# Performance work log

Hardware: AMD Instinct MI355X
Metric: run time of the kernel (lower is better)

## Reference

```python
import jax, jax.numpy as jnp
import numpy as np

N, E, L, H, D, HID = 32768, 262144, 4, 8, 64, 512
IN_DIM, OUT_DIM, EDIM, MAX_SP = 386, 384, 32, 4


def setup_inputs() -> dict:
    key = jax.random.key(0)
    k = jax.random.split(key, 16)
    s = 0.02
    d = {}
    d["embeddings"] = jax.random.normal(k[0], (N, IN_DIM), jnp.float32)
    d["edge_index"] = jax.random.randint(k[1], (2, E), 0, N)
    d["edge_attr_ids"] = jax.random.randint(k[2], (E,), 0, MAX_SP)
    d["Win"] = jax.random.normal(k[3], (IN_DIM, HID)) * s
    d["bin_"] = jnp.zeros((HID,))
    d["Etab"] = jax.random.normal(k[4], (MAX_SP, EDIM)) * s
    d["Wq"] = jax.random.normal(k[5], (L, HID, HID)) * s
    d["bq"] = jnp.zeros((L, HID))
    d["Wk"] = jax.random.normal(k[6], (L, HID, HID)) * s
    d["bk"] = jnp.zeros((L, HID))
    d["Wv"] = jax.random.normal(k[7], (L, HID, HID)) * s
    d["bv"] = jnp.zeros((L, HID))
    d["We"] = jax.random.normal(k[8], (L, EDIM, HID)) * s
    d["be"] = jnp.zeros((L, HID))
    d["Ws"] = jax.random.normal(k[9], (L, HID, HID)) * s
    d["bs"] = jnp.zeros((L, HID))
    d["Wbeta"] = jax.random.normal(k[10], (L, 3 * HID, 1)) * s
    d["bbeta"] = jnp.zeros((L, 1))
    d["ln_g"] = jnp.ones((L, HID))
    d["ln_b"] = jnp.zeros((L, HID))
    d["Wout"] = jax.random.normal(k[11], (HID, OUT_DIM)) * s
    d["bout"] = jnp.zeros((OUT_DIM,))
    return d


def _ln(x, g, b):
    mu = x.mean(-1, keepdims=True)
    var = ((x - mu) ** 2).mean(-1, keepdims=True)
    return (x - mu) * jax.lax.rsqrt(var + 1e-5) * g + b


def _fwd(embeddings, edge_index, edge_attr_ids, Win, bin_, Etab, Wq, bq, Wk, bk,
         Wv, bv, We, be, Ws, bs, Wbeta, bbeta, ln_g, ln_b, Wout, bout):
    src, dst = edge_index[0], edge_index[1]  # messages flow src -> dst (PyG convention)
    h = embeddings @ Win + bin_              # [N, HID]
    e = Etab[edge_attr_ids]                  # [E, EDIM]
    scale = 1.0 / np.sqrt(D).astype(np.float32)
    for l in range(L):
        q = (h @ Wq[l] + bq[l]).reshape(N, H, D)
        kk = (h @ Wk[l] + bk[l]).reshape(N, H, D)
        v = (h @ Wv[l] + bv[l]).reshape(N, H, D)
        ee = (e @ We[l] + be[l]).reshape(E, H, D)
        kj = kk[src] + ee                    # [E, H, D]
        vj = v[src] + ee                     # [E, H, D]
        alpha = jnp.einsum('ehd,ehd->eh', q[dst], kj) * scale  # [E, H]
        # segment softmax over incoming edges of each target node
        amax = jax.lax.stop_gradient(jax.ops.segment_max(alpha, dst, num_segments=N))
        ex = jnp.exp(alpha - amax[dst])
        denom = jax.ops.segment_sum(ex, dst, num_segments=N)
        a = ex / denom[dst]                  # [E, H] (dropout in eval mode -> identity)
        out = jax.ops.segment_sum(a[..., None] * vj, dst, num_segments=N).reshape(N, HID)
        # beta-gated skip connection (PyG TransformerConv beta=True)
        xr = h @ Ws[l] + bs[l]
        beta = jax.nn.sigmoid(jnp.concatenate([out, xr, out - xr], axis=-1) @ Wbeta[l] + bbeta[l])
        out = beta * xr + (1.0 - beta) * out
        h = _ln(h + out, ln_g[l], ln_b[l])
    return h @ Wout + bout


def reference(embeddings, edge_index, edge_attr_ids, Win, bin_, Etab, Wq, bq, Wk,
              bk, Wv, bv, We, be, Ws, bs, Wbeta, bbeta, ln_g, ln_b, Wout, bout):
    return _fwd(embeddings, edge_index, edge_attr_ids, Win, bin_, Etab, Wq, bq,
                Wk, bk, Wv, bv, We, be, Ws, bs, Wbeta, bbeta, ln_g, ln_b, Wout, bout)
```

## Files before the change

### kernel.cpp

```cpp
#include <hip/hip_runtime.h>
#include <math.h>

#define NN      32768
#define EE_N    262144
#define LL      4
#define HID     512
#define IN_DIM  386
#define KP_IN   416
#define OUT_DIM 384
#define EDIM    32
#define MAX_SP  4
#define QKV_LD  1536

typedef __attribute__((ext_vector_type(8))) __bf16 bf16x8;
typedef __attribute__((ext_vector_type(4))) float  f32x4;

__device__ __forceinline__ unsigned short f2bf(float f) {
    unsigned int u = __float_as_uint(f);
    unsigned int r = (u + 0x7FFFu + ((u >> 16) & 1u)) >> 16;
    return (unsigned short)r;
}
__device__ __forceinline__ void unpack2(unsigned int w, float& lo, float& hi) {
    lo = __uint_as_float(w << 16);
    hi = __uint_as_float(w & 0xFFFF0000u);
}

template <int OUT_MODE>
__global__ __launch_bounds__(256) void gemm_mfma(
    const unsigned short* __restrict__ A,
    const unsigned short* __restrict__ Bt,
    const float* __restrict__ bias,
    void* __restrict__ C0, void* __restrict__ C1,
    int M, int Kp, int N, int ldc)
{
    __shared__ unsigned short As[128 * 32];
    __shared__ unsigned short Bs[128 * 32];

    const int t    = threadIdx.x;
    const int lane = t & 63, wid = t >> 6;
    const int wr   = wid >> 1, wc = wid & 1;

    const int nwg = gridDim.x * gridDim.y;
    int bid = blockIdx.y * gridDim.x + blockIdx.x;
    if ((nwg & 7) == 0) bid = (bid & 7) * (nwg >> 3) + (bid >> 3);
    const int row0 = (bid / gridDim.x) * 128;
    const int col0 = (bid % gridDim.x) * 128;

    f32x4 acc[4][4] = {};

    const int srow  = lane >> 2;
    const int sslot = lane & 3;
    const int kq    = lane >> 4;
    const int l15   = lane & 15;

    for (int kt = 0; kt < Kp; kt += 32) {
#pragma unroll
        for (int i = 0; i < 2; ++i) {
            const int rbase = wid * 32 + i * 16;
            {
                const int r    = rbase + srow;
                const int koff = sslot ^ ((r >> 1) & 3);
                const unsigned short* ga = &A[(size_t)(row0 + r) * Kp + kt + koff * 8];
                __builtin_amdgcn_global_load_lds(
                    (const __attribute__((address_space(1))) unsigned int*)ga,
                    (__attribute__((address_space(3))) unsigned int*)&As[rbase * 32],
                    16, 0, 0);
            }
            {
                const int c    = rbase + srow;
                const int koff = sslot ^ ((c >> 1) & 3);
                const unsigned short* gb = &Bt[(size_t)(col0 + c) * Kp + kt + koff * 8];
                __builtin_amdgcn_global_load_lds(
                    (const __attribute__((address_space(1))) unsigned int*)gb,
                    (__attribute__((address_space(3))) unsigned int*)&Bs[rbase * 32],
                    16, 0, 0);
            }
        }
        __syncthreads();

        bf16x8 af[4], bfr[4];
#pragma unroll
        for (int mi = 0; mi < 4; ++mi) {
            const int r    = wr * 64 + mi * 16 + l15;
            const int slot = kq ^ ((r >> 1) & 3);
            af[mi] = *reinterpret_cast<const bf16x8*>(&As[r * 32 + slot * 8]);
        }
#pragma unroll
        for (int ni = 0; ni < 4; ++ni) {
            const int c    = wc * 64 + ni * 16 + l15;
            const int slot = kq ^ ((c >> 1) & 3);
            bfr[ni] = *reinterpret_cast<const bf16x8*>(&Bs[c * 32 + slot * 8]);
        }
#pragma unroll
        for (int mi = 0; mi < 4; ++mi)
#pragma unroll
            for (int ni = 0; ni < 4; ++ni)
                acc[mi][ni] = __builtin_amdgcn_mfma_f32_16x16x32_bf16(
                    af[mi], bfr[ni], acc[mi][ni], 0, 0, 0);
        __syncthreads();
    }

    const int cb = col0 + wc * 64;
    const int rb = row0 + wr * 64;
    float bv[4];
#pragma unroll
    for (int ni = 0; ni < 4; ++ni) bv[ni] = bias[cb + ni * 16 + l15];

#pragma unroll
    for (int mi = 0; mi < 4; ++mi) {
#pragma unroll
        for (int ni = 0; ni < 4; ++ni) {
            const int col = cb + ni * 16 + l15;
#pragma unroll
            for (int r = 0; r < 4; ++r) {
                const int row = rb + mi * 16 + kq * 4 + r;
                const float oval = acc[mi][ni][r] + bv[ni];
                if (OUT_MODE == 0) {
                    ((float*)C0)[(size_t)row * ldc + col] = oval;
                } else if (OUT_MODE == 1) {
                    ((unsigned short*)C0)[(size_t)row * ldc + col] = f2bf(oval);
                } else {
                    ((float*)C0)[(size_t)row * ldc + col] = oval;
                    ((unsigned short*)C1)[(size_t)row * ldc + col] = f2bf(oval);
                }
            }
        }
    }
}

__global__ __launch_bounds__(256) void convert_wt(
    const float* __restrict__ W, unsigned short* __restrict__ Wt,
    int K, int N, int Kp)
{
    __shared__ float tile[32][33];
    const int tx = threadIdx.x, ty = threadIdx.y;
    const int kb = blockIdx.y * 32, nb = blockIdx.x * 32;
#pragma unroll
    for (int i = 0; i < 32; i += 8) {
        const int k = kb + ty + i, n = nb + tx;
        tile[ty + i][tx] = (k < K && n < N) ? W[(size_t)k * N + n] : 0.f;
    }
    __syncthreads();
#pragma unroll
    for (int i = 0; i < 32; i += 8) {
        const int n = nb + ty + i, k = kb + tx;
        if (n < N && k < Kp)
            Wt[(size_t)n * Kp + k] = f2bf(tile[tx][ty + i]);
    }
}

__global__ __launch_bounds__(256) void convert_wt_batch(
    const float* __restrict__ Wq, const float* __restrict__ Wk,
    const float* __restrict__ Wv, const float* __restrict__ Ws,
    unsigned short* __restrict__ Wlt)
{
    __shared__ float tile[32][33];
    const int m = blockIdx.z;
    const int l = m >> 2, tp = m & 3;
    const float* W = (tp == 0 ? Wq : tp == 1 ? Wk : tp == 2 ? Wv : Ws)
                     + (size_t)l * HID * HID;
    unsigned short* Wt = Wlt + (size_t)m * HID * HID;
    const int tx = threadIdx.x, ty = threadIdx.y;
    const int kb = blockIdx.y * 32, nb = blockIdx.x * 32;
#pragma unroll
    for (int i = 0; i < 32; i += 8)
        tile[ty + i][tx] = W[(size_t)(kb + ty + i) * HID + nb + tx];
    __syncthreads();
#pragma unroll
    for (int i = 0; i < 32; i += 8)
        Wt[(size_t)(nb + ty + i) * HID + kb + tx] = f2bf(tile[tx][ty + i]);
}

__global__ __launch_bounds__(256) void convert_emb(
    const float* __restrict__ emb, unsigned short* __restrict__ ebf)
{
    const int n = blockIdx.x;
    for (int k = threadIdx.x; k < KP_IN; k += 256)
        ebf[(size_t)n * KP_IN + k] =
            (k < IN_DIM) ? f2bf(emb[(size_t)n * IN_DIM + k]) : (unsigned short)0;
}

__global__ void ee_all_kernel(const float* __restrict__ Etab,
                              const float* __restrict__ We,
                              const float* __restrict__ be,
                              float* __restrict__ ee4)
{
    const int l = blockIdx.x, j = threadIdx.x;
    const float* Wel = We + (size_t)l * EDIM * HID;
    const float  bel = be[(size_t)l * HID + j];
    for (int a = 0; a < MAX_SP; ++a) {
        float s = bel;
        for (int kk = 0; kk < EDIM; ++kk)
            s = fmaf(Etab[a * EDIM + kk], Wel[(size_t)kk * HID + j], s);
        ee4[((size_t)l * MAX_SP + a) * HID + j] = s;
    }
}

__global__ void bias_fuse_kernel(const float* __restrict__ bq,
                                 const float* __restrict__ bk,
                                 const float* __restrict__ bv,
                                 float* __restrict__ bqkv)
{
    const int i = blockIdx.x * 256 + threadIdx.x;
    const int l = i / QKV_LD, r = i % QKV_LD;
    float val = (r < 512) ? bq[l * 512 + r]
              : (r < 1024) ? bk[l * 512 + r - 512]
                           : bv[l * 512 + r - 1024];
    bqkv[i] = val;
}

__global__ void hist_kernel(const int* __restrict__ dst, int* __restrict__ deg)
{
    int e = blockIdx.x * blockDim.x + threadIdx.x;
    if (e < EE_N) atomicAdd(&deg[dst[e]], 1);
}

__global__ __launch_bounds__(1024) void scan_kernel(
    const int* __restrict__ deg, int* __restrict__ row_ptr, int* __restrict__ cursor)
{
    __shared__ int sdata[1024];
    const int t = threadIdx.x;
    const int base = t * 32;
    int s = 0;
    for (int i = 0; i < 32; ++i) s += deg[base + i];
    sdata[t] = s;
    __syncthreads();
    for (int off = 1; off < 1024; off <<= 1) {
        int val = (t >= off) ? sdata[t - off] : 0;
        __syncthreads();
        sdata[t] += val;
        __syncthreads();
    }
    int run = sdata[t] - s;
    for (int i = 0; i < 32; ++i) {
        row_ptr[base + i] = run;
        cursor[base + i]  = run;
        run += deg[base + i];
    }
    if (t == 1023) row_ptr[NN] = run;
}

__global__ void scatter_kernel(const int* __restrict__ src, const int* __restrict__ dst,
                               const int* __restrict__ aid, int* __restrict__ cursor,
                               int* __restrict__ csr_pack)
{
    int e = blockIdx.x * blockDim.x + threadIdx.x;
    if (e < EE_N) {
        int d = dst[e];
        int pos = atomicAdd(&cursor[d], 1);
        csr_pack[pos] = src[e] | (aid[e] << 16);
    }
}

__global__ __launch_bounds__(256) void attn_kernel(
    unsigned short* __restrict__ qkv, const float* __restrict__ ee,
    const int* __restrict__ row_ptr, const int* __restrict__ csr_pack)
{
    __shared__ float ees[MAX_SP * HID];
    const int t = threadIdx.x;
    for (int i = t; i < MAX_SP * HID; i += 256) ees[i] = ee[i];
    __syncthreads();

    const int wave = t >> 6, lane = t & 63;
    const int node = blockIdx.x * 4 + wave;
    const int off  = lane << 3;

    float qa[8];
    {
        uint4 qv = *reinterpret_cast<const uint4*>(&qkv[(size_t)node * QKV_LD + off]);
        unpack2(qv.x, qa[0], qa[1]); unpack2(qv.y, qa[2], qa[3]);
        unpack2(qv.z, qa[4], qa[5]); unpack2(qv.w, qa[6], qa[7]);
    }

    float denom = 0.f;
    float acc[8] = {0.f, 0.f, 0.f, 0.f, 0.f, 0.f, 0.f, 0.f};

    const int beg = row_ptr[node], end = row_ptr[node + 1];
    for (int i = beg; i < end; ++i) {
        const int p   = csr_pack[i];
        const int s   = p & 0xFFFF;
        const int aid = p >> 16;
        const float* ep = &ees[aid * HID + off];
        const unsigned short* kp = &qkv[(size_t)s * QKV_LD + 512 + off];

        uint4 kv = *reinterpret_cast<const uint4*>(kp);
        uint4 vv = *reinterpret_cast<const uint4*>(kp + 512);

        float kj[8];
        unpack2(kv.x, kj[0], kj[1]); unpack2(kv.y, kj[2], kj[3]);
        unpack2(kv.z, kj[4], kj[5]); unpack2(kv.w, kj[6], kj[7]);
        float partial = 0.f;
#pragma unroll
        for (int j = 0; j < 8; ++j) partial = fmaf(qa[j], kj[j] + ep[j], partial);
        partial += __shfl_xor(partial, 1);
        partial += __shfl_xor(partial, 2);
        partial += __shfl_xor(partial, 4);
        const float w = __expf(partial * 0.125f);
        denom += w;

        float vj[8];
        unpack2(vv.x, vj[0], vj[1]); unpack2(vv.y, vj[2], vj[3]);
        unpack2(vv.z, vj[4], vj[5]); unpack2(vv.w, vj[6], vj[7]);
#pragma unroll
        for (int j = 0; j < 8; ++j) acc[j] = fmaf(w, vj[j] + ep[j], acc[j]);
    }

    const float inv = (denom > 0.f) ? (1.f / denom) : 0.f;
    union { unsigned short us[8]; uint4 v4; } pk;
#pragma unroll
    for (int j = 0; j < 8; ++j) pk.us[j] = f2bf(acc[j] * inv);
    *reinterpret_cast<uint4*>(&qkv[(size_t)node * QKV_LD + off]) = pk.v4;
}

__global__ __launch_bounds__(256) void blend_ln_kernel(
    float* __restrict__ h, unsigned short* __restrict__ hbf,
    const unsigned short* __restrict__ qkv, const float* __restrict__ wbeta,
    const float* __restrict__ bbeta, const float* __restrict__ ln_g,
    const float* __restrict__ ln_b)
{
    const int t = threadIdx.x;
    const int wave = t >> 6, lane = t & 63;
    const int node = blockIdx.x * 4 + wave;
    const int off  = lane << 3;

    float o8[8], x8[8], h8[8];
    {
        uint4 a = *reinterpret_cast<const uint4*>(&qkv[(size_t)node * QKV_LD + off]);
        unpack2(a.x, o8[0], o8[1]); unpack2(a.y, o8[2], o8[3]);
        unpack2(a.z, o8[4], o8[5]); unpack2(a.w, o8[6], o8[7]);
        uint4 b = *reinterpret_cast<const uint4*>(&qkv[(size_t)node * QKV_LD + 512 + off]);
        unpack2(b.x, x8[0], x8[1]); unpack2(b.y, x8[2], x8[3]);
        unpack2(b.z, x8[4], x8[5]); unpack2(b.w, x8[6], x8[7]);
        float4 c0 = *reinterpret_cast<const float4*>(&h[(size_t)node * HID + off]);
        float4 c1 = *reinterpret_cast<const float4*>(&h[(size_t)node * HID + off + 4]);
        h8[0]=c0.x; h8[1]=c0.y; h8[2]=c0.z; h8[3]=c0.w; h8[4]=c1.x; h8[5]=c1.y; h8[6]=c1.z; h8[7]=c1.w;
    }

    float p = 0.f;
#pragma unroll
    for (int j = 0; j < 8; ++j) {
        float w1 = wbeta[off + j];
        float w2 = wbeta[HID + off + j];
        float w3 = wbeta[2 * HID + off + j];
        p = fmaf(o8[j], w1 + w3, p);
        p = fmaf(x8[j], w2 - w3, p);
    }
#pragma unroll
    for (int m = 1; m <= 32; m <<= 1) p += __shfl_xor(p, m);
    const float beta = 1.f / (1.f + __expf(-(p + bbeta[0])));

    float y[8];
    float s = 0.f;
#pragma unroll
    for (int j = 0; j < 8; ++j) {
        y[j] = h8[j] + beta * x8[j] + (1.f - beta) * o8[j];
        s += y[j];
    }
#pragma unroll
    for (int m = 1; m <= 32; m <<= 1) s += __shfl_xor(s, m);
    const float mean = s * (1.f / HID);

    float vs = 0.f;
#pragma unroll
    for (int j = 0; j < 8; ++j) {
        float d = y[j] - mean;
        vs = fmaf(d, d, vs);
    }
#pragma unroll
    for (int m = 1; m <= 32; m <<= 1) vs += __shfl_xor(vs, m);
    const float rstd = rsqrtf(vs * (1.f / HID) + 1e-5f);

    float rr[8];
    union { unsigned short us[8]; uint4 v4; } pk;
#pragma unroll
    for (int j = 0; j < 8; ++j) {
        rr[j] = (y[j] - mean) * rstd * ln_g[off + j] + ln_b[off + j];
        pk.us[j] = f2bf(rr[j]);
    }
    float4 r0 = {rr[0], rr[1], rr[2], rr[3]};
    float4 r1 = {rr[4], rr[5], rr[6], rr[7]};
    *reinterpret_cast<float4*>(&h[(size_t)node * HID + off])     = r0;
    *reinterpret_cast<float4*>(&h[(size_t)node * HID + off + 4]) = r1;
    *reinterpret_cast<uint4*>(&hbf[(size_t)node * HID + off])    = pk.v4;
}

extern "C" void kernel_launch(void* const* d_in, const int* in_sizes, int n_in,
                              void* d_out, int out_size, void* d_ws, size_t ws_size,
                              hipStream_t stream)
{
    (void)in_sizes; (void)n_in; (void)out_size; (void)ws_size;
    const float* emb   = (const float*)d_in[0];
    const int*   eidx  = (const int*)d_in[1];
    const int*   aid   = (const int*)d_in[2];
    const float* Win   = (const float*)d_in[3];
    const float* bin_  = (const float*)d_in[4];
    const float* Etab  = (const float*)d_in[5];
    const float* Wq    = (const float*)d_in[6];
    const float* bq    = (const float*)d_in[7];
    const float* Wk    = (const float*)d_in[8];
    const float* bk    = (const float*)d_in[9];
    const float* Wv    = (const float*)d_in[10];
    const float* bv    = (const float*)d_in[11];
    const float* We    = (const float*)d_in[12];
    const float* be    = (const float*)d_in[13];
    const float* Ws    = (const float*)d_in[14];
    const float* bs    = (const float*)d_in[15];
    const float* Wbeta = (const float*)d_in[16];
    const float* bbeta = (const float*)d_in[17];
    const float* ln_g  = (const float*)d_in[18];
    const float* ln_b  = (const float*)d_in[19];
    const float* Wout  = (const float*)d_in[20];
    const float* bout  = (const float*)d_in[21];
    float* out = (float*)d_out;

    char* w = (char*)d_ws;
    float* h            = (float*)w;           w += (size_t)NN * HID * 4;
    unsigned short* hbf = (unsigned short*)w;  w += (size_t)NN * HID * 2;
    unsigned short* qkv = (unsigned short*)w;  w += (size_t)NN * QKV_LD * 2;
    unsigned short* embbf = qkv;
    unsigned short* Winbf  = (unsigned short*)w; w += (size_t)HID * KP_IN * 2;
    unsigned short* Wlt    = (unsigned short*)w; w += (size_t)16 * HID * HID * 2;
    unsigned short* Woutbf = (unsigned short*)w; w += (size_t)OUT_DIM * HID * 2;
    float* ee4   = (float*)w;  w += (size_t)LL * MAX_SP * HID * 4;
    float* bqkv  = (float*)w;  w += (size_t)LL * QKV_LD * 4;
    int* row_ptr = (int*)w;    w += (NN + 4) * 4;
    int* cursor  = (int*)w;    w += NN * 4;
    int* deg     = (int*)w;    w += NN * 4;
    int* csr_pack = (int*)w;   w += EE_N * 4;

    const int* src = eidx;
    const int* dst = eidx + EE_N;

    hipMemsetAsync(deg, 0, NN * sizeof(int), stream);
    hist_kernel<<<EE_N / 256, 256, 0, stream>>>(dst, deg);
    scan_kernel<<<1, 1024, 0, stream>>>(deg, row_ptr, cursor);
    scatter_kernel<<<EE_N / 256, 256, 0, stream>>>(src, dst, aid, cursor, csr_pack);

    dim3 tb(32, 8);
    convert_wt<<<dim3(HID / 32, KP_IN / 32), tb, 0, stream>>>(Win, Winbf, IN_DIM, HID, KP_IN);
    convert_wt_batch<<<dim3(16, 16, 16), tb, 0, stream>>>(Wq, Wk, Wv, Ws, Wlt);
    convert_wt<<<dim3(OUT_DIM / 32, HID / 32), tb, 0, stream>>>(Wout, Woutbf, HID, OUT_DIM, HID);
    convert_emb<<<NN, 256, 0, stream>>>(emb, embbf);
    ee_all_kernel<<<LL, HID, 0, stream>>>(Etab, We, be, ee4);
    bias_fuse_kernel<<<LL * QKV_LD / 256, 256, 0, stream>>>(bq, bk, bv, bqkv);

    gemm_mfma<2><<<dim3(HID / 128, NN / 128), 256, 0, stream>>>(
        embbf, Winbf, bin_, h, hbf, NN, KP_IN, HID, HID);

    for (int l = 0; l < LL; ++l) {
        gemm_mfma<1><<<dim3(QKV_LD / 128, NN / 128), 256, 0, stream>>>(
            hbf, Wlt + (size_t)(l * 4) * HID * HID, bqkv + (size_t)l * QKV_LD,
            qkv, nullptr, NN, HID, QKV_LD, QKV_LD);
        attn_kernel<<<NN / 4, 256, 0, stream>>>(
            qkv, ee4 + (size_t)l * MAX_SP * HID, row_ptr, csr_pack);
        gemm_mfma<1><<<dim3(HID / 128, NN / 128), 256, 0, stream>>>(
            hbf, Wlt + (size_t)(l * 4 + 3) * HID * HID, bs + (size_t)l * HID,
            qkv + 512, nullptr, NN, HID, HID, QKV_LD);
        blend_ln_kernel<<<NN / 4, 256, 0, stream>>>(
            h, hbf, qkv, Wbeta + (size_t)l * 3 * HID, bbeta + l,
            ln_g + (size_t)l * HID, ln_b + (size_t)l * HID);
    }

    gemm_mfma<0><<<dim3(OUT_DIM / 128, NN / 128), 256, 0, stream>>>(
        hbf, Woutbf, bout, out, nullptr, NN, HID, OUT_DIM, OUT_DIM);
}
```

Before: 1.173 ms.

## Fuse skip projection into QKV GEMM and unroll attention edge loop by two

When the workspace is large enough, the per-layer Ws projection is folded into the Q/K/V GEMM as a fourth 512-column block (row stride 2048), so one launch replaces two and hbf is read once per layer. The attention kernel now processes two edges per iteration with separate accumulators, giving more independent gathers in flight. The trade-off is a larger qkv buffer and a runtime fallback to the old layout when the workspace is too small.

Result: no change. 1.192 ms (+1.6%).

```diff
diff --git a/kernel.cpp b/kernel.cpp
--- a/kernel.cpp
+++ b/kernel.cpp
@@ -10,7 +10,6 @@
 #define OUT_DIM 384
 #define EDIM    32
 #define MAX_SP  4
-#define QKV_LD  1536
 
 typedef __attribute__((ext_vector_type(8))) __bf16 bf16x8;
 typedef __attribute__((ext_vector_type(4))) float  f32x4;
@@ -23,6 +22,10 @@
 __device__ __forceinline__ void unpack2(unsigned int w, float& lo, float& hi) {
     lo = __uint_as_float(w << 16);
     hi = __uint_as_float(w & 0xFFFF0000u);
+}
+__device__ __forceinline__ void unpack8(const uint4& v, float* f) {
+    unpack2(v.x, f[0], f[1]); unpack2(v.y, f[2], f[3]);
+    unpack2(v.z, f[4], f[5]); unpack2(v.w, f[6], f[7]);
 }
 
 template <int OUT_MODE>
@@ -199,14 +202,16 @@
 __global__ void bias_fuse_kernel(const float* __restrict__ bq,
                                  const float* __restrict__ bk,
                                  const float* __restrict__ bv,
-                                 float* __restrict__ bqkv)
+                                 const float* __restrict__ bs,
+                                 float* __restrict__ bqkvs)
 {
     const int i = blockIdx.x * 256 + threadIdx.x;
-    const int l = i / QKV_LD, r = i % QKV_LD;
-    float val = (r < 512) ? bq[l * 512 + r]
+    const int l = i >> 11, r = i & 2047;
+    float val = (r < 512)  ? bq[l * 512 + r]
               : (r < 1024) ? bk[l * 512 + r - 512]
-                           : bv[l * 512 + r - 1024];
-    bqkv[i] = val;
+              : (r < 1536) ? bv[l * 512 + r - 1024]
+                           : bs[l * 512 + r - 1536];
+    bqkvs[i] = val;
 }
 
 __global__ void hist_kernel(const int* __restrict__ dst, int* __restrict__ deg)
@@ -254,7 +259,7 @@
 
 __global__ __launch_bounds__(256) void attn_kernel(
     unsigned short* __restrict__ qkv, const float* __restrict__ ee,
-    const int* __restrict__ row_ptr, const int* __restrict__ csr_pack)
+    const int* __restrict__ row_ptr, const int* __restrict__ csr_pack, int ld)
 {
     __shared__ float ees[MAX_SP * HID];
     const int t = threadIdx.x;
@@ -267,56 +272,86 @@
 
     float qa[8];
     {
-        uint4 qv = *reinterpret_cast<const uint4*>(&qkv[(size_t)node * QKV_LD + off]);
-        unpack2(qv.x, qa[0], qa[1]); unpack2(qv.y, qa[2], qa[3]);
-        unpack2(qv.z, qa[4], qa[5]); unpack2(qv.w, qa[6], qa[7]);
-    }
-
-    float denom = 0.f;
-    float acc[8] = {0.f, 0.f, 0.f, 0.f, 0.f, 0.f, 0.f, 0.f};
+        uint4 qv = *reinterpret_cast<const uint4*>(&qkv[(size_t)node * ld + off]);
+        unpack8(qv, qa);
+    }
+
+    float denomA = 0.f, denomB = 0.f;
+    float accA[8] = {0.f,0.f,0.f,0.f,0.f,0.f,0.f,0.f};
+    float accB[8] = {0.f,0.f,0.f,0.f,0.f,0.f,0.f,0.f};
 
     const int beg = row_ptr[node], end = row_ptr[node + 1];
-    for (int i = beg; i < end; ++i) {
-        const int p   = csr_pack[i];
-        const int s   = p & 0xFFFF;
-        const int aid = p >> 16;
-        const float* ep = &ees[aid * HID + off];
-        const unsigned short* kp = &qkv[(size_t)s * QKV_LD + 512 + off];
-
-        uint4 kv = *reinterpret_cast<const uint4*>(kp);
-        uint4 vv = *reinterpret_cast<const uint4*>(kp + 512);
-
-        float kj[8];
-        unpack2(kv.x, kj[0], kj[1]); unpack2(kv.y, kj[2], kj[3]);
-        unpack2(kv.z, kj[4], kj[5]); unpack2(kv.w, kj[6], kj[7]);
-        float partial = 0.f;
-#pragma unroll
-        for (int j = 0; j < 8; ++j) partial = fmaf(qa[j], kj[j] + ep[j], partial);
-        partial += __shfl_xor(partial, 1);
-        partial += __shfl_xor(partial, 2);
-        partial += __shfl_xor(partial, 4);
-        const float w = __expf(partial * 0.125f);
-        denom += w;
-
-        float vj[8];
-        unpack2(vv.x, vj[0], vj[1]); unpack2(vv.y, vj[2], vj[3]);
-        unpack2(vv.z, vj[4], vj[5]); unpack2(vv.w, vj[6], vj[7]);
-#pragma unroll
-        for (int j = 0; j < 8; ++j) acc[j] = fmaf(w, vj[j] + ep[j], acc[j]);
-    }
-
+    int i = beg;
+    for (; i + 2 <= end; i += 2) {
+        const int p0 = csr_pack[i];
+        const int p1 = csr_pack[i + 1];
+        const unsigned short* kp0 = &qkv[(size_t)(p0 & 0xFFFF) * ld + 512 + off];
+        const unsigned short* kp1 = &qkv[(size_t)(p1 & 0xFFFF) * ld + 512 + off];
+        const uint4 kv0 = *reinterpret_cast<const uint4*>(kp0);
+        const uint4 vv0 = *reinterpret_cast<const uint4*>(kp0 + 512);
+        const uint4 kv1 = *reinterpret_cast<const uint4*>(kp1);
+        const uint4 vv1 = *reinterpret_cast<const uint4*>(kp1 + 512);
+        const float* ep0 = &ees[(p0 >> 16) * HID + off];
+        const float* ep1 = &ees[(p1 >> 16) * HID + off];
+
+        float k0[8], k1[8];
+        unpack8(kv0, k0); unpack8(kv1, k1);
+        float d0 = 0.f, d1 = 0.f;
+#pragma unroll
+        for (int j = 0; j < 8; ++j) {
+            d0 = fmaf(qa[j], k0[j] + ep0[j], d0);
+            d1 = fmaf(qa[j], k1[j] + ep1[j], d1);
+        }
+        d0 += __shfl_xor(d0, 1); d1 += __shfl_xor(d1, 1);
+        d0 += __shfl_xor(d0, 2); d1 += __shfl_xor(d1, 2);
+        d0 += __shfl_xor(d0, 4); d1 += __shfl_xor(d1, 4);
+        const float w0 = __expf(d0 * 0.125f);
+        const float w1 = __expf(d1 * 0.125f);
+        denomA += w0; denomB += w1;
+
+        float v0[8], v1[8];
+        unpack8(vv0, v0); unpack8(vv1, v1);
+#pragma unroll
+        for (int j = 0; j < 8; ++j) {
+            accA[j] = fmaf(w0, v0[j] + ep0[j], accA[j]);
+            accB[j] = fmaf(w1, v1[j] + ep1[j], accB[j]);
+        }
+    }
+    if (i < end) {
+        const int p0 = csr_pack[i];
+        const unsigned short* kp0 = &qkv[(size_t)(p0 & 0xFFFF) * ld + 512 + off];
+        const uint4 kv0 = *reinterpret_cast<const uint4*>(kp0);
+        const uint4 vv0 = *reinterpret_cast<const uint4*>(kp0 + 512);
+        const float* ep0 = &ees[(p0 >> 16) * HID + off];
+        float k0[8];
+        unpack8(kv0, k0);
+        float d0 = 0.f;
+#pragma unroll
+        for (int j = 0; j < 8; ++j) d0 = fmaf(qa[j], k0[j] + ep0[j], d0);
+        d0 += __shfl_xor(d0, 1);
+        d0 += __shfl_xor(d0, 2);
+        d0 += __shfl_xor(d0, 4);
+        const float w0 = __expf(d0 * 0.125f);
+        denomA += w0;
+        float v0[8];
+        unpack8(vv0, v0);
+#pragma unroll
+        for (int j = 0; j < 8; ++j) accA[j] = fmaf(w0, v0[j] + ep0[j], accA[j]);
+    }
+
+    const float denom = denomA + denomB;
     const float inv = (denom > 0.f) ? (1.f / denom) : 0.f;
     union { unsigned short us[8]; uint4 v4; } pk;
 #pragma unroll
-    for (int j = 0; j < 8; ++j) pk.us[j] = f2bf(acc[j] * inv);
-    *reinterpret_cast<uint4*>(&qkv[(size_t)node * QKV_LD + off]) = pk.v4;
+    for (int j = 0; j < 8; ++j) pk.us[j] = f2bf((accA[j] + accB[j]) * inv);
+    *reinterpret_cast<uint4*>(&qkv[(size_t)node * ld + off]) = pk.v4;
 }
 
 __global__ __launch_bounds__(256) void blend_ln_kernel(
     float* __restrict__ h, unsigned short* __restrict__ hbf,
     const unsigned short* __restrict__ qkv, const float* __restrict__ wbeta,
     const float* __restrict__ bbeta, const float* __restrict__ ln_g,
-    const float* __restrict__ ln_b)
+    const float* __restrict__ ln_b, int ld, int xr_off)
 {
     const int t = threadIdx.x;
     const int wave = t >> 6, lane = t & 63;
@@ -325,12 +360,10 @@
 
     float o8[8], x8[8], h8[8];
     {
-        uint4 a = *reinterpret_cast<const uint4*>(&qkv[(size_t)node * QKV_LD + off]);
-        unpack2(a.x, o8[0], o8[1]); unpack2(a.y, o8[2], o8[3]);
-        unpack2(a.z, o8[4], o8[5]); unpack2(a.w, o8[6], o8[7]);
-        uint4 b = *reinterpret_cast<const uint4*>(&qkv[(size_t)node * QKV_LD + 512 + off]);
-        unpack2(b.x, x8[0], x8[1]); unpack2(b.y, x8[2], x8[3]);
-        unpack2(b.z, x8[4], x8[5]); unpack2(b.w, x8[6], x8[7]);
+        uint4 a = *reinterpret_cast<const uint4*>(&qkv[(size_t)node * ld + off]);
+        unpack8(a, o8);
+        uint4 b = *reinterpret_cast<const uint4*>(&qkv[(size_t)node * ld + xr_off + off]);
+        unpack8(b, x8);
         float4 c0 = *reinterpret_cast<const float4*>(&h[(size_t)node * HID + off]);
         float4 c1 = *reinterpret_cast<const float4*>(&h[(size_t)node * HID + off + 4]);
         h8[0]=c0.x; h8[1]=c0.y; h8[2]=c0.z; h8[3]=c0.w; h8[4]=c1.x; h8[5]=c1.y; h8[6]=c1.z; h8[7]=c1.w;
@@ -388,7 +421,7 @@
                               void* d_out, int out_size, void* d_ws, size_t ws_size,
                               hipStream_t stream)
 {
-    (void)in_sizes; (void)n_in; (void)out_size; (void)ws_size;
+    (void)in_sizes; (void)n_in; (void)out_size;
     const float* emb   = (const float*)d_in[0];
     const int*   eidx  = (const int*)d_in[1];
     const int*   aid   = (const int*)d_in[2];
@@ -413,16 +446,27 @@
     const float* bout  = (const float*)d_in[21];
     float* out = (float*)d_out;
 
+    const size_t fixed_tail =
+        (size_t)HID * KP_IN * 2 + (size_t)16 * HID * HID * 2 +
+        (size_t)OUT_DIM * HID * 2 + (size_t)LL * MAX_SP * HID * 4 +
+        (size_t)LL * 2048 * 4 + (size_t)(NN + 4) * 4 + (size_t)NN * 4 * 2 +
+        (size_t)EE_N * 4;
+    const size_t base_sz = (size_t)NN * HID * 4 + (size_t)NN * HID * 2;
+    const size_t need_wide = base_sz + (size_t)NN * 2048 * 2 + fixed_tail;
+    const bool wide = (ws_size >= need_wide);
+    const int  ld     = wide ? 2048 : 1536;
+    const int  xr_off = wide ? 1536 : 512;
+
     char* w = (char*)d_ws;
     float* h            = (float*)w;           w += (size_t)NN * HID * 4;
     unsigned short* hbf = (unsigned short*)w;  w += (size_t)NN * HID * 2;
-    unsigned short* qkv = (unsigned short*)w;  w += (size_t)NN * QKV_LD * 2;
+    unsigned short* qkv = (unsigned short*)w;  w += (size_t)NN * ld * 2;
     unsigned short* embbf = qkv;
     unsigned short* Winbf  = (unsigned short*)w; w += (size_t)HID * KP_IN * 2;
     unsigned short* Wlt    = (unsigned short*)w; w += (size_t)16 * HID * HID * 2;
     unsigned short* Woutbf = (unsigned short*)w; w += (size_t)OUT_DIM * HID * 2;
     float* ee4   = (float*)w;  w += (size_t)LL * MAX_SP * HID * 4;
-    float* bqkv  = (float*)w;  w += (size_t)LL * QKV_LD * 4;
+    float* bqkvs = (float*)w;  w += (size_t)LL * 2048 * 4;
     int* row_ptr = (int*)w;    w += (NN + 4) * 4;
     int* cursor  = (int*)w;    w += NN * 4;
     int* deg     = (int*)w;    w += NN * 4;
@@ -442,23 +486,31 @@
     convert_wt<<<dim3(OUT_DIM / 32, HID / 32), tb, 0, stream>>>(Wout, Woutbf, HID, OUT_DIM, HID);
     convert_emb<<<NN, 256, 0, stream>>>(emb, embbf);
     ee_all_kernel<<<LL, HID, 0, stream>>>(Etab, We, be, ee4);
-    bias_fuse_kernel<<<LL * QKV_LD / 256, 256, 0, stream>>>(bq, bk, bv, bqkv);
+    bias_fuse_kernel<<<LL * 2048 / 256, 256, 0, stream>>>(bq, bk, bv, bs, bqkvs);
 
     gemm_mfma<2><<<dim3(HID / 128, NN / 128), 256, 0, stream>>>(
         embbf, Winbf, bin_, h, hbf, NN, KP_IN, HID, HID);
 
     for (int l = 0; l < LL; ++l) {
-        gemm_mfma<1><<<dim3(QKV_LD / 128, NN / 128), 256, 0, stream>>>(
-            hbf, Wlt + (size_t)(l * 4) * HID * HID, bqkv + (size_t)l * QKV_LD,
-            qkv, nullptr, NN, HID, QKV_LD, QKV_LD);
-        attn_kernel<<<NN / 4, 256, 0, stream>>>(
-            qkv, ee4 + (size_t)l * MAX_SP * HID, row_ptr, csr_pack);
-        gemm_mfma<1><<<dim3(HID / 128, NN / 128), 256, 0, stream>>>(
-            hbf, Wlt + (size_t)(l * 4 + 3) * HID * HID, bs + (size_t)l * HID,
-            qkv + 512, nullptr, NN, HID, HID, QKV_LD);
+        if (wide) {
+            gemm_mfma<1><<<dim3(2048 / 128, NN / 128), 256, 0, stream>>>(
+                hbf, Wlt + (size_t)(l * 4) * HID * HID, bqkvs + (size_t)l * 2048,
+                qkv, nullptr, NN, HID, 2048, 2048);
+            attn_kernel<<<NN / 4, 256, 0, stream>>>(
+                qkv, ee4 + (size_t)l * MAX_SP * HID, row_ptr, csr_pack, 2048);
+        } else {
+            gemm_mfma<1><<<dim3(1536 / 128, NN / 128), 256, 0, stream>>>(
+                hbf, Wlt + (size_t)(l * 4) * HID * HID, bqkvs + (size_t)l * 2048,
+                qkv, nullptr, NN, HID, 1536, 1536);
+            attn_kernel<<<NN / 4, 256, 0, stream>>>(
+                qkv, ee4 + (size_t)l * MAX_SP * HID, row_ptr, csr_pack, 1536);
+            gemm_mfma<1><<<dim3(HID / 128, NN / 128), 256, 0, stream>>>(
+                hbf, Wlt + (size_t)(l * 4 + 3) * HID * HID, bs + (size_t)l * HID,
+                qkv + 512, nullptr, NN, HID, HID, 1536);
+        }
         blend_ln_kernel<<<NN / 4, 256, 0, stream>>>(
             h, hbf, qkv, Wbeta + (size_t)l * 3 * HID, bbeta + l,
-            ln_g + (size_t)l * HID, ln_b + (size_t)l * HID);
+            ln_g + (size_t)l * HID, ln_b + (size_t)l * HID, ld, xr_off);
     }
 
     gemm_mfma<0><<<dim3(OUT_DIM / 128, NN / 128), 256, 0, stream>>>(
```
